# Performance work log

Hardware: AMD Instinct MI355X
Metric: run time of the kernel (lower is better)

Reference implementation:

```python
import jax, jax.numpy as jnp
import numpy as np

N_NODES = 50000
NEG_SLOPE = 0.2  # PyG GATConv default


def gat_layer(x, src, dst, W, a_src, a_dst, b, concat):
    """PyG-style GATConv (eval mode, self-loops already in src/dst).
    x: [N, Fin], W: [Fin, H*C], a_src/a_dst: [H, C], b: [H*C] or [C]."""
    N = x.shape[0]
    H, C = a_src.shape
    h = (x @ W).reshape(N, H, C)                      # [N,H,C]
    alpha_s = jnp.einsum('nhc,hc->nh', h, a_src)      # [N,H]
    alpha_d = jnp.einsum('nhc,hc->nh', h, a_dst)
    e = jax.nn.leaky_relu(alpha_s[src] + alpha_d[dst], NEG_SLOPE)  # [E,H]
    # segment softmax over incoming edges of each dst node
    m = jax.ops.segment_max(e, dst, num_segments=N)   # [N,H]
    e = jnp.exp(e - m[dst])
    denom = jax.ops.segment_sum(e, dst, num_segments=N)  # [N,H]
    msg = e[:, :, None] * h[src]                      # [E,H,C] (largest intermediate)
    out = jax.ops.segment_sum(msg, dst, num_segments=N)
    out = out / jnp.maximum(denom[:, :, None], 1e-16) # [N,H,C]
    out = out.reshape(N, H * C) if concat else out.mean(axis=1)
    return out + b


def setup_inputs() -> dict:
    key = jax.random.key(0)
    ks = jax.random.split(key, 10)
    N, E = N_NODES, 1600000
    Fin, Chid, Cout, H = 3, 32, 16, 4
    s = lambda *sh: 1.0 / np.sqrt(sh[-1])
    return {
        'x': jax.random.normal(ks[0], (N, Fin), dtype=jnp.float32),
        'edge_index': jax.random.randint(ks[1], (2, E), 0, N, dtype=jnp.int64),
        'W1': jax.random.normal(ks[2], (Fin, H * Chid), dtype=jnp.float32) * s(Fin),
        'att_src1': jax.random.normal(ks[3], (H, Chid), dtype=jnp.float32) * s(Chid),
        'att_dst1': jax.random.normal(ks[4], (H, Chid), dtype=jnp.float32) * s(Chid),
        'b1': jnp.zeros((H * Chid,), dtype=jnp.float32),
        'W2': jax.random.normal(ks[5], (H * Chid, Cout), dtype=jnp.float32) * s(H * Chid),
        'att_src2': jax.random.normal(ks[6], (1, Cout), dtype=jnp.float32) * s(Cout),
        'att_dst2': jax.random.normal(ks[7], (1, Cout), dtype=jnp.float32) * s(Cout),
        'b2': jnp.zeros((Cout,), dtype=jnp.float32),
    }


def reference(x, edge_index, W1, att_src1, att_dst1, b1, W2, att_src2, att_dst2, b2):
    N = x.shape[0]
    loops = jnp.arange(N, dtype=edge_index.dtype)
    src = jnp.concatenate([edge_index[0], loops])
    dst = jnp.concatenate([edge_index[1], loops])
    h = gat_layer(x, src, dst, W1, att_src1, att_dst1, b1, concat=True)  # [N,128]
    h = jax.nn.elu(h)  # dropout is identity in eval mode
    out = gat_layer(h, src, dst, W2, att_src2, att_dst2, b2, concat=False)  # [N,16]
    return out
```

## Files before the change

### kernel.cpp

```cpp
#include <hip/hip_runtime.h>

#define LRELU(v) ((v) > 0.f ? (v) : 0.2f * (v))
#define MAXNB 512
#define BCAP 8192
#define WCAP (BCAP + 128)
#define MS_CHUNK 8192

__global__ void __launch_bounds__(256) k_h1(const float* __restrict__ x,
                                            const float* __restrict__ W1,
                                            const float* __restrict__ aws,
                                            const float* __restrict__ awd,
                                            const int* __restrict__ ei,
                                            float* __restrict__ rec2,
                                            float* __restrict__ ad1,
                                            int* __restrict__ gcur,
                                            int* __restrict__ flag, int nb, int N) {
    int t = threadIdx.x;
    if (blockIdx.x == 0) {
        for (int i = t; i < nb; i += 256) gcur[i] = i * BCAP;
        if (t < 64) {
            int a = ei[2 * t + 1];
            int b = ei[2 * (t + 64) + 1];
            unsigned long long any = __ballot((a | b) != 0);
            if (t == 0) *flag = (any == 0ull) ? 1 : 0;
        }
    }
    int n = blockIdx.x * 2 + (t >> 7);
    int f = t & 127;
    if (n >= N) return;
    float x0 = x[n * 3 + 0], x1 = x[n * 3 + 1], x2 = x[n * 3 + 2];
    float h = fmaf(x0, W1[f], fmaf(x1, W1[128 + f], x2 * W1[256 + f]));
    float ps = h * aws[f];
    float pd = h * awd[f];
#pragma unroll
    for (int m = 1; m < 32; m <<= 1) {
        ps += __shfl_xor(ps, m);
        pd += __shfl_xor(pd, m);
    }
    int head = f >> 5;
    if ((f & 31) == 0) {
        *(float4*)(rec2 + ((size_t)n * 4 + head) * 4) = make_float4(ps, x0, x1, x2);
        ad1[n * 4 + head] = pd;
    }
}

__global__ void __launch_bounds__(256) k_msplit(const int* __restrict__ ei, long long E,
                                                const int* __restrict__ flag,
                                                int* __restrict__ gcur,
                                                unsigned* __restrict__ bstage) {
    __shared__ unsigned stage[MS_CHUNK];
    __shared__ int h[MAXNB], lbase[MAXNB], lcur[MAXNB];
    int t = threadIdx.x;
    for (int i = t; i < MAXNB; i += 256) h[i] = 0;
    __syncthreads();
    long long beg = (long long)blockIdx.x * MS_CHUNK;
    int cnt = (int)min((long long)MS_CHUNK, E - beg);
    int is64 = *flag;
    for (int k = t; k < cnt; k += 256) {
        long long i = beg + k;
        int s, d;
        if (is64) {
            s = (int)((const long long*)ei)[i];
            d = (int)((const long long*)ei)[E + i];
        } else {
            s = ei[i];
            d = ei[E + i];
        }
        stage[k] = (unsigned)s | ((unsigned)d << 16);
        atomicAdd(&h[d >> 7], 1);
    }
    __syncthreads();
    for (int b = t; b < MAXNB; b += 256) {
        lcur[b] = 0;
        if (h[b]) lbase[b] = atomicAdd(&gcur[b], h[b]);
    }
    __syncthreads();
    for (int k = t; k < cnt; k += 256) {
        unsigned pk = stage[k];
        int b = (int)(pk >> 23);
        int idx = lbase[b] + atomicAdd(&lcur[b], 1);
        if (idx < (b + 1) * BCAP) bstage[idx] = pk;
    }
}

__global__ void __launch_bounds__(256) k_bucket(const unsigned* __restrict__ bstage,
                                                const int* __restrict__ gcur,
                                                int* __restrict__ beg,
                                                int* __restrict__ endo,
                                                int* __restrict__ ssrc, int N) {
    __shared__ int nc[128];
    __shared__ int sscan[128];
    __shared__ int lcur[128];
    int b = blockIdx.x, t = threadIdx.x;
    if (t < 128) nc[t] = 0;
    __syncthreads();
    int base = b * BCAP;
    int c = min(gcur[b], (b + 1) * BCAP) - base;
    for (int i = t; i < c; i += 256)
        atomicAdd(&nc[(bstage[base + i] >> 16) & 127], 1);
    __syncthreads();
    int node = b * 128 + (t & 127);
    int v = 0;
    if (t < 128) {
        v = (node < N) ? nc[t] + 1 : 0;
        sscan[t] = v;
    }
    __syncthreads();
#pragma unroll
    for (int off = 1; off < 128; off <<= 1) {
        int add = (t < 128 && t >= off) ? sscan[t - off] : 0;
        __syncthreads();
        if (t < 128) sscan[t] += add;
        __syncthreads();
    }
    int sbase = b * WCAP;
    if (t < 128 && node < N) {
        int o = sbase + sscan[t] - v;
        beg[node] = o;
        endo[node] = o + v;
        ssrc[o] = node;
        lcur[t] = o + 1;
    }
    __syncthreads();
    for (int i = t; i < c; i += 256) {
        unsigned pk = bstage[base + i];
        int p = atomicAdd(&lcur[(pk >> 16) & 127], 1);
        ssrc[p] = (int)(pk & 0xFFFFu);
    }
}

__global__ void __launch_bounds__(256) k_gat1w(const float* __restrict__ rec2,
                                               const float* __restrict__ ad1,
                                               const int* __restrict__ beg,
                                               const int* __restrict__ endo,
                                               const int* __restrict__ ssrc,
                                               const float* __restrict__ W1,
                                               const float* __restrict__ b1,
                                               const float* __restrict__ W2,
                                               const float* __restrict__ aws2,
                                               const float* __restrict__ awd2,
                                               float* __restrict__ h2w,
                                               float* __restrict__ as2,
                                               float* __restrict__ ad2, int N) {
    __shared__ float sW1[384], sb1[128], sW2[128 * 16];
    __shared__ float shx[16][132];
    int t = threadIdx.x;
    for (int i = t; i < 384; i += 256) sW1[i] = W1[i];
    if (t < 128) sb1[t] = b1[t];
    for (int i = t; i < 2048; i += 256) sW2[i] = W2[i];

    int nl = t >> 4;
    int g = t & 15;
    int lane = t & 63;
    int n = blockIdx.x * 16 + nl;
    int slot = g >> 2, head = g & 3;

    float t0 = 0.f, t1 = 0.f, t2 = 0.f, ds = 0.f;
    if (n < N) {
        int e0 = beg[n], e1 = endo[n];
        float ad = ad1[n * 4 + head];
        for (int e = e0 + slot; e < e1; e += 4) {
            int s = ssrc[e];
            float4 rv = *(const float4*)(rec2 + ((size_t)s * 4 + head) * 4);
            float w = __expf(LRELU(rv.x + ad));
            ds += w;
            t0 = fmaf(w, rv.y, t0);
            t1 = fmaf(w, rv.z, t1);
            t2 = fmaf(w, rv.w, t2);
        }
    }
#pragma unroll
    for (int msk = 4; msk < 16; msk <<= 1) {
        t0 += __shfl_xor(t0, msk);
        t1 += __shfl_xor(t1, msk);
        t2 += __shfl_xor(t2, msk);
        ds += __shfl_xor(ds, msk);
    }
    float dinv = 1.f / fmaxf(ds, 1e-16f);

    int srcl = (lane & 48) | (g >> 2);
    float u0 = __shfl(t0, srcl);
    float u1 = __shfl(t1, srcl);
    float u2 = __shfl(t2, srcl);
    float ui = __shfl(dinv, srcl);
    __syncthreads();
    int f0 = g * 8;
#pragma unroll
    for (int j = 0; j < 8; ++j) {
        int f = f0 + j;
        float o = fmaf(fmaf(u0, sW1[f], fmaf(u1, sW1[128 + f], u2 * sW1[256 + f])), ui, sb1[f]);
        shx[nl][f] = (o > 0.f) ? o : __expf(o) - 1.f;
    }
    __syncthreads();

    int c = g;
    const float4* hr4 = (const float4*)shx[nl];
    float acc = 0.f;
#pragma unroll 8
    for (int k4 = 0; k4 < 32; ++k4) {
        float4 hv = hr4[k4];
        acc = fmaf(hv.x, sW2[(k4 * 4 + 0) * 16 + c], acc);
        acc = fmaf(hv.y, sW2[(k4 * 4 + 1) * 16 + c], acc);
        acc = fmaf(hv.z, sW2[(k4 * 4 + 2) * 16 + c], acc);
        acc = fmaf(hv.w, sW2[(k4 * 4 + 3) * 16 + c], acc);
    }
    if (n < N) {
        h2w[n * 16 + c] = acc;
        float ps = acc * aws2[c];
        float pd = acc * awd2[c];
#pragma unroll
        for (int m = 1; m < 16; m <<= 1) {
            ps += __shfl_xor(ps, m);
            pd += __shfl_xor(pd, m);
        }
        if (c == 0) {
            as2[n] = ps;
            ad2[n] = pd;
        }
    }
}

__global__ void __launch_bounds__(256) k_gat2(const float* __restrict__ h2w,
                                              const float* __restrict__ as2,
                                              const float* __restrict__ ad2,
                                              const int* __restrict__ beg,
                                              const int* __restrict__ endo,
                                              const int* __restrict__ ssrc,
                                              const float* __restrict__ b2,
                                              float* __restrict__ out, int N) {
    int t = threadIdx.x;
    int nl = t >> 4, g = t & 15;
    int n = blockIdx.x * 16 + nl;
    if (n >= N) return;
    int slot = g >> 2, c4 = g & 3;
    int e0 = beg[n], e1 = endo[n];
    float ad = ad2[n];

    float4 acc = {0.f, 0.f, 0.f, 0.f};
    float ds = 0.f;
    for (int e = e0 + slot; e < e1; e += 4) {
        int s = ssrc[e];
        float w = __expf(LRELU(as2[s] + ad));
        ds += w;
        const float4 hv = *(const float4*)(h2w + (size_t)s * 16 + c4 * 4);
        acc.x = fmaf(w, hv.x, acc.x);
        acc.y = fmaf(w, hv.y, acc.y);
        acc.z = fmaf(w, hv.z, acc.z);
        acc.w = fmaf(w, hv.w, acc.w);
    }
#pragma unroll
    for (int msk = 4; msk < 16; msk <<= 1) {
        acc.x += __shfl_xor(acc.x, msk);
        acc.y += __shfl_xor(acc.y, msk);
        acc.z += __shfl_xor(acc.z, msk);
        acc.w += __shfl_xor(acc.w, msk);
        ds += __shfl_xor(ds, msk);
    }
    if (slot == 0) {
        float inv = 1.f / fmaxf(ds, 1e-16f);
        float4 bq = ((const float4*)b2)[c4];
        float4 o;
        o.x = fmaf(acc.x, inv, bq.x);
        o.y = fmaf(acc.y, inv, bq.y);
        o.z = fmaf(acc.z, inv, bq.z);
        o.w = fmaf(acc.w, inv, bq.w);
        *(float4*)(out + (size_t)n * 16 + c4 * 4) = o;
    }
}

extern "C" void kernel_launch(void* const* d_in, const int* in_sizes, int n_in,
                              void* d_out, int out_size, void* d_ws, size_t ws_size,
                              hipStream_t stream) {
    const float* x    = (const float*)d_in[0];
    const int*   ei   = (const int*)d_in[1];
    const float* W1   = (const float*)d_in[2];
    const float* aws1 = (const float*)d_in[3];
    const float* awd1 = (const float*)d_in[4];
    const float* b1   = (const float*)d_in[5];
    const float* W2   = (const float*)d_in[6];
    const float* aws2 = (const float*)d_in[7];
    const float* awd2 = (const float*)d_in[8];
    const float* b2   = (const float*)d_in[9];
    float* out = (float*)d_out;

    const int N = in_sizes[0] / 3;
    const long long E = in_sizes[1] / 2;
    const int NB = (N + 127) / 128;

    char* w = (char*)d_ws;
    auto alloc = [&](size_t bytes) {
        char* p = w;
        w += (bytes + 255) & ~(size_t)255;
        return p;
    };
    float*    rec2   = (float*)alloc((size_t)N * 16 * 4);
    float*    ad1    = (float*)alloc((size_t)N * 4 * 4);
    float*    h2w    = (float*)alloc((size_t)N * 16 * 4);
    float*    as2    = (float*)alloc((size_t)N * 4);
    float*    ad2    = (float*)alloc((size_t)N * 4);
    int*      beg    = (int*)alloc((size_t)N * 4);
    int*      endo   = (int*)alloc((size_t)N * 4);
    int*      ssrc   = (int*)alloc((size_t)NB * WCAP * 4);
    unsigned* bstage = (unsigned*)alloc((size_t)NB * BCAP * 4);
    int*      gcur   = (int*)alloc((size_t)NB * 4);
    int*      flag   = (int*)alloc(4);

    k_h1<<<(N + 1) / 2, 256, 0, stream>>>(x, W1, aws1, awd1, ei, rec2, ad1,
                                          gcur, flag, NB, N);
    k_msplit<<<(int)((E + MS_CHUNK - 1) / MS_CHUNK), 256, 0, stream>>>(ei, E, flag, gcur, bstage);
    k_bucket<<<NB, 256, 0, stream>>>(bstage, gcur, beg, endo, ssrc, N);
    k_gat1w<<<(N + 15) / 16, 256, 0, stream>>>(rec2, ad1, beg, endo, ssrc, W1, b1,
                                               W2, aws2, awd2, h2w, as2, ad2, N);
    k_gat2<<<(N + 15) / 16, 256, 0, stream>>>(h2w, as2, ad2, beg, endo, ssrc, b2, out, N);
}
```

Baseline: 111.5 us.

## Fuse bucket CSR build with layer-1 aggregation using shared-memory atomics

Merges the bucketing kernel and the layer-1 GAT aggregation kernel into one 512-thread kernel per 128-node bucket. Layer-1 edge weights and weighted sums are accumulated straight from the staged edge list into shared-memory accumulators with atomics, instead of a later pass re-reading the CSR. The per-node record is compacted to 8 floats (4 head scores plus x). This saves a kernel launch and a pass over ssrc, but adds heavy LDS atomic contention and only 391 blocks of work. Results may also differ slightly because the atomic summation order is nondeterministic.

```diff
diff --git a/kernel.cpp b/kernel.cpp
--- a/kernel.cpp
+++ b/kernel.cpp
@@ -11,7 +11,7 @@
                                             const float* __restrict__ aws,
                                             const float* __restrict__ awd,
                                             const int* __restrict__ ei,
-                                            float* __restrict__ rec2,
+                                            float* __restrict__ rec,
                                             float* __restrict__ ad1,
                                             int* __restrict__ gcur,
                                             int* __restrict__ flag, int nb, int N) {
@@ -39,9 +39,10 @@
     }
     int head = f >> 5;
     if ((f & 31) == 0) {
-        *(float4*)(rec2 + ((size_t)n * 4 + head) * 4) = make_float4(ps, x0, x1, x2);
+        rec[n * 8 + head] = ps;
         ad1[n * 4 + head] = pd;
     }
+    if (f < 3) rec[n * 8 + 4 + f] = x[n * 3 + f];
 }
 
 __global__ void __launch_bounds__(256) k_msplit(const int* __restrict__ ei, long long E,
@@ -83,23 +84,75 @@
     }
 }
 
-__global__ void __launch_bounds__(256) k_bucket(const unsigned* __restrict__ bstage,
-                                                const int* __restrict__ gcur,
-                                                int* __restrict__ beg,
-                                                int* __restrict__ endo,
-                                                int* __restrict__ ssrc, int N) {
-    __shared__ int nc[128];
-    __shared__ int sscan[128];
-    __shared__ int lcur[128];
+__global__ void __launch_bounds__(512) k_fuse1(const unsigned* __restrict__ bstage,
+                                               const int* __restrict__ gcur,
+                                               const float* __restrict__ rec,
+                                               const float* __restrict__ ad1,
+                                               const float* __restrict__ W1,
+                                               const float* __restrict__ b1,
+                                               const float* __restrict__ W2,
+                                               const float* __restrict__ aws2,
+                                               const float* __restrict__ awd2,
+                                               int* __restrict__ beg,
+                                               int* __restrict__ endo,
+                                               int* __restrict__ ssrc,
+                                               float* __restrict__ h2w,
+                                               float* __restrict__ as2,
+                                               float* __restrict__ ad2, int N) {
+    __shared__ float acc[16][128];
+    __shared__ float ad1s[4][128];
+    __shared__ int nc[128], sscan[128], lcur[128];
+    __shared__ float sW1[384], sb1[128], sW2[128 * 16];
+    __shared__ float shx[32][132];
+
     int b = blockIdx.x, t = threadIdx.x;
-    if (t < 128) nc[t] = 0;
-    __syncthreads();
+    int node0 = b * 128;
     int base = b * BCAP;
-    int c = min(gcur[b], (b + 1) * BCAP) - base;
-    for (int i = t; i < c; i += 256)
-        atomicAdd(&nc[(bstage[base + i] >> 16) & 127], 1);
-    __syncthreads();
-    int node = b * 128 + (t & 127);
+    int cnt = min(gcur[b], base + BCAP) - base;
+
+    for (int i = t; i < 384; i += 512) sW1[i] = W1[i];
+    for (int i = t; i < 2048; i += 512) sW2[i] = W2[i];
+    if (t < 128) { sb1[t] = b1[t]; nc[t] = 0; }
+    for (int i = t; i < 2048; i += 512) ((float*)acc)[i] = 0.f;
+    {
+        int n = node0 + (t >> 2);
+        ad1s[t & 3][t >> 2] = (n < N) ? ad1[(size_t)n * 4 + (t & 3)] : 0.f;
+    }
+    __syncthreads();
+
+    if (t < 128 && node0 + t < N) {
+        const float4 a4 = *(const float4*)(rec + (size_t)(node0 + t) * 8);
+        const float4 x4 = *(const float4*)(rec + (size_t)(node0 + t) * 8 + 4);
+        float av[4] = {a4.x, a4.y, a4.z, a4.w};
+#pragma unroll
+        for (int h = 0; h < 4; ++h) {
+            float w = __expf(LRELU(av[h] + ad1s[h][t]));
+            atomicAdd(&acc[h * 4 + 0][t], w * x4.x);
+            atomicAdd(&acc[h * 4 + 1][t], w * x4.y);
+            atomicAdd(&acc[h * 4 + 2][t], w * x4.z);
+            atomicAdd(&acc[h * 4 + 3][t], w);
+        }
+    }
+    for (int i = t; i < cnt; i += 512) {
+        unsigned pk = bstage[base + i];
+        int s = (int)(pk & 0xFFFFu);
+        int d = (int)((pk >> 16) & 127u);
+        atomicAdd(&nc[d], 1);
+        const float4 a4 = *(const float4*)(rec + (size_t)s * 8);
+        const float4 x4 = *(const float4*)(rec + (size_t)s * 8 + 4);
+        float av[4] = {a4.x, a4.y, a4.z, a4.w};
+#pragma unroll
+        for (int h = 0; h < 4; ++h) {
+            float w = __expf(LRELU(av[h] + ad1s[h][d]));
+            atomicAdd(&acc[h * 4 + 0][d], w * x4.x);
+            atomicAdd(&acc[h * 4 + 1][d], w * x4.y);
+            atomicAdd(&acc[h * 4 + 2][d], w * x4.z);
+            atomicAdd(&acc[h * 4 + 3][d], w);
+        }
+    }
+    __syncthreads();
+
+    int node = node0 + (t & 127);
     int v = 0;
     if (t < 128) {
         v = (node < N) ? nc[t] + 1 : 0;
@@ -122,101 +175,57 @@
         lcur[t] = o + 1;
     }
     __syncthreads();
-    for (int i = t; i < c; i += 256) {
+    for (int i = t; i < cnt; i += 512) {
         unsigned pk = bstage[base + i];
         int p = atomicAdd(&lcur[(pk >> 16) & 127], 1);
         ssrc[p] = (int)(pk & 0xFFFFu);
     }
-}
-
-__global__ void __launch_bounds__(256) k_gat1w(const float* __restrict__ rec2,
-                                               const float* __restrict__ ad1,
-                                               const int* __restrict__ beg,
-                                               const int* __restrict__ endo,
-                                               const int* __restrict__ ssrc,
-                                               const float* __restrict__ W1,
-                                               const float* __restrict__ b1,
-                                               const float* __restrict__ W2,
-                                               const float* __restrict__ aws2,
-                                               const float* __restrict__ awd2,
-                                               float* __restrict__ h2w,
-                                               float* __restrict__ as2,
-                                               float* __restrict__ ad2, int N) {
-    __shared__ float sW1[384], sb1[128], sW2[128 * 16];
-    __shared__ float shx[16][132];
-    int t = threadIdx.x;
-    for (int i = t; i < 384; i += 256) sW1[i] = W1[i];
-    if (t < 128) sb1[t] = b1[t];
-    for (int i = t; i < 2048; i += 256) sW2[i] = W2[i];
-
-    int nl = t >> 4;
-    int g = t & 15;
-    int lane = t & 63;
-    int n = blockIdx.x * 16 + nl;
-    int slot = g >> 2, head = g & 3;
-
-    float t0 = 0.f, t1 = 0.f, t2 = 0.f, ds = 0.f;
-    if (n < N) {
-        int e0 = beg[n], e1 = endo[n];
-        float ad = ad1[n * 4 + head];
-        for (int e = e0 + slot; e < e1; e += 4) {
-            int s = ssrc[e];
-            float4 rv = *(const float4*)(rec2 + ((size_t)s * 4 + head) * 4);
-            float w = __expf(LRELU(rv.x + ad));
-            ds += w;
-            t0 = fmaf(w, rv.y, t0);
-            t1 = fmaf(w, rv.z, t1);
-            t2 = fmaf(w, rv.w, t2);
-        }
-    }
-#pragma unroll
-    for (int msk = 4; msk < 16; msk <<= 1) {
-        t0 += __shfl_xor(t0, msk);
-        t1 += __shfl_xor(t1, msk);
-        t2 += __shfl_xor(t2, msk);
-        ds += __shfl_xor(ds, msk);
-    }
-    float dinv = 1.f / fmaxf(ds, 1e-16f);
-
-    int srcl = (lane & 48) | (g >> 2);
-    float u0 = __shfl(t0, srcl);
-    float u1 = __shfl(t1, srcl);
-    float u2 = __shfl(t2, srcl);
-    float ui = __shfl(dinv, srcl);
-    __syncthreads();
-    int f0 = g * 8;
-#pragma unroll
-    for (int j = 0; j < 8; ++j) {
-        int f = f0 + j;
-        float o = fmaf(fmaf(u0, sW1[f], fmaf(u1, sW1[128 + f], u2 * sW1[256 + f])), ui, sb1[f]);
-        shx[nl][f] = (o > 0.f) ? o : __expf(o) - 1.f;
-    }
-    __syncthreads();
-
-    int c = g;
-    const float4* hr4 = (const float4*)shx[nl];
-    float acc = 0.f;
+
+    int nl = t >> 4, g = t & 15;
+#pragma unroll
+    for (int tile = 0; tile < 4; ++tile) {
+        int d = tile * 32 + nl;
+        int n2 = node0 + d;
+        int head = g >> 2;
+        float u0 = acc[head * 4 + 0][d];
+        float u1 = acc[head * 4 + 1][d];
+        float u2 = acc[head * 4 + 2][d];
+        float ds = acc[head * 4 + 3][d];
+        float ui = 1.f / fmaxf(ds, 1e-16f);
+        int f0 = g * 8;
+#pragma unroll
+        for (int j = 0; j < 8; ++j) {
+            int f = f0 + j;
+            float o = fmaf(fmaf(u0, sW1[f], fmaf(u1, sW1[128 + f], u2 * sW1[256 + f])), ui, sb1[f]);
+            shx[nl][f] = (o > 0.f) ? o : __expf(o) - 1.f;
+        }
+        __syncthreads();
+        int c = g;
+        const float4* hr4 = (const float4*)shx[nl];
+        float a2 = 0.f;
 #pragma unroll 8
-    for (int k4 = 0; k4 < 32; ++k4) {
-        float4 hv = hr4[k4];
-        acc = fmaf(hv.x, sW2[(k4 * 4 + 0) * 16 + c], acc);
-        acc = fmaf(hv.y, sW2[(k4 * 4 + 1) * 16 + c], acc);
-        acc = fmaf(hv.z, sW2[(k4 * 4 + 2) * 16 + c], acc);
-        acc = fmaf(hv.w, sW2[(k4 * 4 + 3) * 16 + c], acc);
-    }
-    if (n < N) {
-        h2w[n * 16 + c] = acc;
-        float ps = acc * aws2[c];
-        float pd = acc * awd2[c];
-#pragma unroll
-        for (int m = 1; m < 16; m <<= 1) {
-            ps += __shfl_xor(ps, m);
-            pd += __shfl_xor(pd, m);
-        }
-        if (c == 0) {
-            as2[n] = ps;
-            ad2[n] = pd;
-        }
+        for (int k4 = 0; k4 < 32; ++k4) {
+            float4 hv = hr4[k4];
+            a2 = fmaf(hv.x, sW2[(k4 * 4 + 0) * 16 + c], a2);
+            a2 = fmaf(hv.y, sW2[(k4 * 4 + 1) * 16 + c], a2);
+            a2 = fmaf(hv.z, sW2[(k4 * 4 + 2) * 16 + c], a2);
+            a2 = fmaf(hv.w, sW2[(k4 * 4 + 3) * 16 + c], a2);
+        }
+        if (n2 < N) {
+            h2w[(size_t)n2 * 16 + c] = a2;
+            float ps = a2 * aws2[c];
+            float pd = a2 * awd2[c];
+#pragma unroll
+            for (int m = 1; m < 16; m <<= 1) {
+                ps += __shfl_xor(ps, m);
+                pd += __shfl_xor(pd, m);
+            }
+            if (c == 0) {
+                as2[n2] = ps;
+                ad2[n2] = pd;
+            }
+        }
+        __syncthreads();
     }
 }
 
@@ -293,7 +302,7 @@
         w += (bytes + 255) & ~(size_t)255;
         return p;
     };
-    float*    rec2   = (float*)alloc((size_t)N * 16 * 4);
+    float*    rec    = (float*)alloc((size_t)N * 8 * 4);
     float*    ad1    = (float*)alloc((size_t)N * 4 * 4);
     float*    h2w    = (float*)alloc((size_t)N * 16 * 4);
     float*    as2    = (float*)alloc((size_t)N * 4);
@@ -305,11 +314,10 @@
     int*      gcur   = (int*)alloc((size_t)NB * 4);
     int*      flag   = (int*)alloc(4);
 
-    k_h1<<<(N + 1) / 2, 256, 0, stream>>>(x, W1, aws1, awd1, ei, rec2, ad1,
+    k_h1<<<(N + 1) / 2, 256, 0, stream>>>(x, W1, aws1, awd1, ei, rec, ad1,
                                           gcur, flag, NB, N);
     k_msplit<<<(int)((E + MS_CHUNK - 1) / MS_CHUNK), 256, 0, stream>>>(ei, E, flag, gcur, bstage);
-    k_bucket<<<NB, 256, 0, stream>>>(bstage, gcur, beg, endo, ssrc, N);
-    k_gat1w<<<(N + 15) / 16, 256, 0, stream>>>(rec2, ad1, beg, endo, ssrc, W1, b1,
-                                               W2, aws2, awd2, h2w, as2, ad2, N);
+    k_fuse1<<<NB, 512, 0, stream>>>(bstage, gcur, rec, ad1, W1, b1, W2,
+                                    aws2, awd2, beg, endo, ssrc, h2w, as2, ad2, N);
     k_gat2<<<(N + 15) / 16, 256, 0, stream>>>(h2w, as2, ad2, beg, endo, ssrc, b2, out, N);
 }
```

Result: slower. 269.5 us (+141.8%).

## Compact per-node record and process all heads per edge in layer-1 aggregation

Applied to the files above, without the earlier changes.

Replaces the per-head 16-float record (alpha_s plus x repeated for each head) with an 8-float record per node holding four alpha_s values and x once. The layer-1 aggregation now gives each of 16 lanes whole edges and computes all four heads from one 32-byte gather, so each lane walks about a quarter as many edges per node. This halves the gathered record size and removes the duplicate index loads per head. In exchange each lane holds 16 accumulators, and the butterfly reduction grows to 16 values over 4 steps, which adds register pressure and shuffle work.

```diff
diff --git a/kernel.cpp b/kernel.cpp
--- a/kernel.cpp
+++ b/kernel.cpp
@@ -11,7 +11,7 @@
                                             const float* __restrict__ aws,
                                             const float* __restrict__ awd,
                                             const int* __restrict__ ei,
-                                            float* __restrict__ rec2,
+                                            float* __restrict__ rec,
                                             float* __restrict__ ad1,
                                             int* __restrict__ gcur,
                                             int* __restrict__ flag, int nb, int N) {
@@ -39,9 +39,10 @@
     }
     int head = f >> 5;
     if ((f & 31) == 0) {
-        *(float4*)(rec2 + ((size_t)n * 4 + head) * 4) = make_float4(ps, x0, x1, x2);
+        rec[n * 8 + head] = ps;
         ad1[n * 4 + head] = pd;
     }
+    if (f < 3) rec[n * 8 + 4 + f] = x[n * 3 + f];
 }
 
 __global__ void __launch_bounds__(256) k_msplit(const int* __restrict__ ei, long long E,
@@ -129,7 +130,7 @@
     }
 }
 
-__global__ void __launch_bounds__(256) k_gat1w(const float* __restrict__ rec2,
+__global__ void __launch_bounds__(256) k_gat1w(const float* __restrict__ rec,
                                                const float* __restrict__ ad1,
                                                const int* __restrict__ beg,
                                                const int* __restrict__ endo,
@@ -151,38 +152,48 @@
 
     int nl = t >> 4;
     int g = t & 15;
-    int lane = t & 63;
     int n = blockIdx.x * 16 + nl;
-    int slot = g >> 2, head = g & 3;
-
-    float t0 = 0.f, t1 = 0.f, t2 = 0.f, ds = 0.f;
+
+    float t0_0 = 0.f, t1_0 = 0.f, t2_0 = 0.f, ds_0 = 0.f;
+    float t0_1 = 0.f, t1_1 = 0.f, t2_1 = 0.f, ds_1 = 0.f;
+    float t0_2 = 0.f, t1_2 = 0.f, t2_2 = 0.f, ds_2 = 0.f;
+    float t0_3 = 0.f, t1_3 = 0.f, t2_3 = 0.f, ds_3 = 0.f;
     if (n < N) {
         int e0 = beg[n], e1 = endo[n];
-        float ad = ad1[n * 4 + head];
-        for (int e = e0 + slot; e < e1; e += 4) {
+        const float4 adv = *(const float4*)(ad1 + (size_t)n * 4);
+        for (int e = e0 + g; e < e1; e += 16) {
             int s = ssrc[e];
-            float4 rv = *(const float4*)(rec2 + ((size_t)s * 4 + head) * 4);
-            float w = __expf(LRELU(rv.x + ad));
-            ds += w;
-            t0 = fmaf(w, rv.y, t0);
-            t1 = fmaf(w, rv.z, t1);
-            t2 = fmaf(w, rv.w, t2);
-        }
-    }
-#pragma unroll
-    for (int msk = 4; msk < 16; msk <<= 1) {
-        t0 += __shfl_xor(t0, msk);
-        t1 += __shfl_xor(t1, msk);
-        t2 += __shfl_xor(t2, msk);
-        ds += __shfl_xor(ds, msk);
-    }
-    float dinv = 1.f / fmaxf(ds, 1e-16f);
-
-    int srcl = (lane & 48) | (g >> 2);
-    float u0 = __shfl(t0, srcl);
-    float u1 = __shfl(t1, srcl);
-    float u2 = __shfl(t2, srcl);
-    float ui = __shfl(dinv, srcl);
+            const float4 a4 = *(const float4*)(rec + (size_t)s * 8);
+            const float4 x4 = *(const float4*)(rec + (size_t)s * 8 + 4);
+            float w;
+            w = __expf(LRELU(a4.x + adv.x));
+            ds_0 += w; t0_0 = fmaf(w, x4.x, t0_0); t1_0 = fmaf(w, x4.y, t1_0); t2_0 = fmaf(w, x4.z, t2_0);
+            w = __expf(LRELU(a4.y + adv.y));
+            ds_1 += w; t0_1 = fmaf(w, x4.x, t0_1); t1_1 = fmaf(w, x4.y, t1_1); t2_1 = fmaf(w, x4.z, t2_1);
+            w = __expf(LRELU(a4.z + adv.z));
+            ds_2 += w; t0_2 = fmaf(w, x4.x, t0_2); t1_2 = fmaf(w, x4.y, t1_2); t2_2 = fmaf(w, x4.z, t2_2);
+            w = __expf(LRELU(a4.w + adv.w));
+            ds_3 += w; t0_3 = fmaf(w, x4.x, t0_3); t1_3 = fmaf(w, x4.y, t1_3); t2_3 = fmaf(w, x4.z, t2_3);
+        }
+    }
+#pragma unroll
+    for (int msk = 1; msk < 16; msk <<= 1) {
+        t0_0 += __shfl_xor(t0_0, msk); t1_0 += __shfl_xor(t1_0, msk);
+        t2_0 += __shfl_xor(t2_0, msk); ds_0 += __shfl_xor(ds_0, msk);
+        t0_1 += __shfl_xor(t0_1, msk); t1_1 += __shfl_xor(t1_1, msk);
+        t2_1 += __shfl_xor(t2_1, msk); ds_1 += __shfl_xor(ds_1, msk);
+        t0_2 += __shfl_xor(t0_2, msk); t1_2 += __shfl_xor(t1_2, msk);
+        t2_2 += __shfl_xor(t2_2, msk); ds_2 += __shfl_xor(ds_2, msk);
+        t0_3 += __shfl_xor(t0_3, msk); t1_3 += __shfl_xor(t1_3, msk);
+        t2_3 += __shfl_xor(t2_3, msk); ds_3 += __shfl_xor(ds_3, msk);
+    }
+    int hs = g >> 2;
+    float u0 = hs == 0 ? t0_0 : hs == 1 ? t0_1 : hs == 2 ? t0_2 : t0_3;
+    float u1 = hs == 0 ? t1_0 : hs == 1 ? t1_1 : hs == 2 ? t1_2 : t1_3;
+    float u2 = hs == 0 ? t2_0 : hs == 1 ? t2_1 : hs == 2 ? t2_2 : t2_3;
+    float dsv = hs == 0 ? ds_0 : hs == 1 ? ds_1 : hs == 2 ? ds_2 : ds_3;
+    float ui = 1.f / fmaxf(dsv, 1e-16f);
+
     __syncthreads();
     int f0 = g * 8;
 #pragma unroll
@@ -205,7 +216,7 @@
         acc = fmaf(hv.w, sW2[(k4 * 4 + 3) * 16 + c], acc);
     }
     if (n < N) {
-        h2w[n * 16 + c] = acc;
+        h2w[(size_t)n * 16 + c] = acc;
         float ps = acc * aws2[c];
         float pd = acc * awd2[c];
 #pragma unroll
@@ -293,7 +304,7 @@
         w += (bytes + 255) & ~(size_t)255;
         return p;
     };
-    float*    rec2   = (float*)alloc((size_t)N * 16 * 4);
+    float*    rec    = (float*)alloc((size_t)N * 8 * 4);
     float*    ad1    = (float*)alloc((size_t)N * 4 * 4);
     float*    h2w    = (float*)alloc((size_t)N * 16 * 4);
     float*    as2    = (float*)alloc((size_t)N * 4);
@@ -305,11 +316,11 @@
     int*      gcur   = (int*)alloc((size_t)NB * 4);
     int*      flag   = (int*)alloc(4);
 
-    k_h1<<<(N + 1) / 2, 256, 0, stream>>>(x, W1, aws1, awd1, ei, rec2, ad1,
+    k_h1<<<(N + 1) / 2, 256, 0, stream>>>(x, W1, aws1, awd1, ei, rec, ad1,
                                           gcur, flag, NB, N);
     k_msplit<<<(int)((E + MS_CHUNK - 1) / MS_CHUNK), 256, 0, stream>>>(ei, E, flag, gcur, bstage);
     k_bucket<<<NB, 256, 0, stream>>>(bstage, gcur, beg, endo, ssrc, N);
-    k_gat1w<<<(N + 15) / 16, 256, 0, stream>>>(rec2, ad1, beg, endo, ssrc, W1, b1,
+    k_gat1w<<<(N + 15) / 16, 256, 0, stream>>>(rec, ad1, beg, endo, ssrc, W1, b1,
                                                W2, aws2, awd2, h2w, as2, ad2, N);
     k_gat2<<<(N + 15) / 16, 256, 0, stream>>>(h2w, as2, ad2, beg, endo, ssrc, b2, out, N);
 }
```

Result: no change. 111.0 us (-0.4%).
